# Kernel tuning notes

Measured on AMD Instinct MI355X. Metric: run time of the kernel, lower is better.

## Reference

```python
import jax, jax.numpy as jnp
import numpy as np

B, N, E, H = 8, 2000, 20, 128


def setup_inputs() -> dict:
    key = jax.random.key(0)
    ks = jax.random.split(key, 9)
    s = 1.0 / np.sqrt(H)
    return {
        "x": jax.random.normal(ks[0], (B, N, H), dtype=jnp.float32),
        "e": jax.random.normal(ks[1], (B, N * E, H), dtype=jnp.float32),
        "Wu": jax.random.uniform(ks[2], (H, H), jnp.float32, -s, s),
        "bu": jax.random.uniform(ks[3], (H,), jnp.float32, -s, s),
        "Wv": jax.random.uniform(ks[4], (H, H), jnp.float32, -s, s),
        "bv": jax.random.uniform(ks[5], (H,), jnp.float32, -s, s),
        "We": jax.random.uniform(ks[6], (H, H), jnp.float32, -s, s),
        "be": jax.random.uniform(ks[7], (H,), jnp.float32, -s, s),
        "edge_index": jax.random.randint(ks[8], (B, N * E), 0, N, dtype=jnp.int32),
        "n_edges": E,
    }


def reference(x, e, Wu, bu, Wv, bv, We, be, edge_index, n_edges):
    b, n, h = x.shape
    Ux = x @ Wu + bu                      # [B, N, H] node self-embedding
    Vx = x @ Wv + bv                      # [B, N, H] neighbor embedding
    Ve = e @ We + be                      # [B, N*E, H] edge embedding
    # softmax over the n_edges axis per (node, channel)
    Ve = jax.nn.softmax(Ve.reshape(b, n, n_edges, h), axis=2)
    # gather neighbor features along node axis via edge_index
    Vx_g = jnp.take_along_axis(Vx, edge_index[..., None], axis=1)  # [B, N*E, H]
    to = (Ve * Vx_g.reshape(b, n, n_edges, h)).sum(axis=2)          # [B, N, H]
    return Ux + to
```

## Files before the change

### kernel.cpp

```cpp
#include <hip/hip_runtime.h>

#define B_   8
#define NN   2000
#define EE   20
#define HH   128
#define BN   (B_*NN)
#define NE   (NN*EE)

typedef unsigned short ushort_t;
typedef __bf16 bf16x8 __attribute__((ext_vector_type(8)));
typedef float  f32x4  __attribute__((ext_vector_type(4)));
typedef float  f4     __attribute__((ext_vector_type(4)));
typedef unsigned short us8 __attribute__((ext_vector_type(8)));
typedef unsigned short us4 __attribute__((ext_vector_type(4)));

union FragU { us8 u; bf16x8 b; };
union Frag32 { unsigned int w[4]; us8 u; bf16x8 b; };

__device__ __forceinline__ float b2f(ushort_t v) {
    union { unsigned int i; float f; } c; c.i = ((unsigned int)v) << 16; return c.f;
}
__device__ __forceinline__ ushort_t f2b(float f) {
    union { float f; unsigned int i; } c; c.f = f;
    unsigned int r = (c.i + 0x7FFFu + ((c.i >> 16) & 1u)) >> 16;
    return (ushort_t)r;
}

__global__ __launch_bounds__(256) void k1_embed(
    const float* __restrict__ x,
    const float* __restrict__ Wu, const float* __restrict__ bu,
    const float* __restrict__ Wv, const float* __restrict__ bv,
    ushort_t* __restrict__ Uxb, ushort_t* __restrict__ Vxb)
{
    const int tid  = threadIdx.x;
    const int lane = tid & 63;
    const int wave = tid >> 6;
    const int wm = wave >> 1, wn = wave & 1;
    const int q  = lane >> 4, ln = lane & 15;
    const int m0 = blockIdx.x * 64;
    const int sel = blockIdx.y;
    const float* W    = sel ? Wv : Wu;
    const float* bias = sel ? bv : bu;
    ushort_t* dst = sel ? Vxb : Uxb;

    FragU af[2][4];
#pragma unroll
    for (int tm = 0; tm < 2; ++tm)
#pragma unroll
        for (int ki = 0; ki < 4; ++ki) {
            const float* p = x + (size_t)(m0 + wm * 32 + tm * 16 + ln) * HH + ki * 32 + q * 8;
            f4 lo = *(const f4*)(p);
            f4 hi = *(const f4*)(p + 4);
            us8 t;
#pragma unroll
            for (int r = 0; r < 4; ++r) { t[r] = f2b(lo[r]); t[r + 4] = f2b(hi[r]); }
            af[tm][ki].u = t;
        }

    FragU bf[4][4];
#pragma unroll
    for (int ki = 0; ki < 4; ++ki)
#pragma unroll
        for (int tn = 0; tn < 4; ++tn) {
            int n = wn * 64 + tn * 16 + ln;
            us8 t;
#pragma unroll
            for (int i = 0; i < 8; ++i) t[i] = f2b(W[(ki * 32 + q * 8 + i) * HH + n]);
            bf[ki][tn].u = t;
        }

    f32x4 acc[2][4];
#pragma unroll
    for (int tm = 0; tm < 2; ++tm)
#pragma unroll
        for (int tn = 0; tn < 4; ++tn) acc[tm][tn] = (f32x4){0.f, 0.f, 0.f, 0.f};

#pragma unroll
    for (int ki = 0; ki < 4; ++ki)
#pragma unroll
        for (int tm = 0; tm < 2; ++tm)
#pragma unroll
            for (int tn = 0; tn < 4; ++tn)
                acc[tm][tn] = __builtin_amdgcn_mfma_f32_16x16x32_bf16(
                    af[tm][ki].b, bf[ki][tn].b, acc[tm][tn], 0, 0, 0);

#pragma unroll
    for (int tn = 0; tn < 4; ++tn) {
        int col = wn * 64 + tn * 16 + ln;
        float bb = bias[col];
#pragma unroll
        for (int tm = 0; tm < 2; ++tm) {
            int rowb = m0 + wm * 32 + tm * 16 + q * 4;
#pragma unroll
            for (int r = 0; r < 4; ++r)
                dst[(size_t)(rowb + r) * HH + col] = f2b(acc[tm][tn][r] + bb);
        }
    }
}

#define CSTR 84

__global__ __launch_bounds__(256, 4) void k2_fused(
    const float* __restrict__ e, const float* __restrict__ We,
    const int* __restrict__ eidx,
    const ushort_t* __restrict__ Uxb, const ushort_t* __restrict__ Vxb,
    float* __restrict__ out)
{
    __shared__ __align__(16) unsigned char smem[40960];

    const int tid  = threadIdx.x;
    const int lane = tid & 63;
    const int wave = tid >> 6;
    const int q  = lane >> 4, ln = lane & 15;

    const int b   = blockIdx.y;
    const int nl0 = blockIdx.x * 4;
    const size_t erow0 = (size_t)b * NE + (size_t)nl0 * EE;

    {
        const int rl = lane >> 5;
        const int sl = lane & 31;
#pragma unroll
        for (int i = 0; i < 10; ++i) {
            const int r0 = wave * 20 + 2 * i;
            const int r  = r0 + rl;
            const int ss = sl ^ (r & 7);
            const float* gp = e + (erow0 + r) * (size_t)HH + (ss << 2);
            __builtin_amdgcn_global_load_lds(
                (const __attribute__((address_space(1))) void*)gp,
                (__attribute__((address_space(3))) void*)(smem + r0 * 512),
                16, 0, 0);
        }
    }

    FragU bfr[4][2];
#pragma unroll
    for (int ki = 0; ki < 4; ++ki)
#pragma unroll
        for (int tn = 0; tn < 2; ++tn) {
            int n = wave * 32 + tn * 16 + ln;
            us8 t;
#pragma unroll
            for (int i = 0; i < 8; ++i) t[i] = f2b(We[(ki * 32 + q * 8 + i) * HH + n]);
            bfr[ki][tn].u = t;
        }

    f32x4 acc[5][2];
#pragma unroll
    for (int tm = 0; tm < 5; ++tm)
#pragma unroll
        for (int tn = 0; tn < 2; ++tn) acc[tm][tn] = (f32x4){0.f, 0.f, 0.f, 0.f};

    asm volatile("s_waitcnt vmcnt(0)" ::: "memory");
    __syncthreads();

    const float* As = (const float*)smem;
#pragma unroll
    for (int ki = 0; ki < 4; ++ki) {
        Frag32 af[5];
#pragma unroll
        for (int tm = 0; tm < 5; ++tm) {
            const int r  = tm * 16 + ln;
            const int sw = r & 7;
            const int s0 = ki * 8 + q * 2;
            f4 lo = *(const f4*)(As + r * 128 + ((s0    ) ^ sw) * 4);
            f4 hi = *(const f4*)(As + r * 128 + ((s0 + 1) ^ sw) * 4);
            asm("v_cvt_pk_bf16_f32 %0, %1, %2" : "=v"(af[tm].w[0]) : "v"(lo[0]), "v"(lo[1]));
            asm("v_cvt_pk_bf16_f32 %0, %1, %2" : "=v"(af[tm].w[1]) : "v"(lo[2]), "v"(lo[3]));
            asm("v_cvt_pk_bf16_f32 %0, %1, %2" : "=v"(af[tm].w[2]) : "v"(hi[0]), "v"(hi[1]));
            asm("v_cvt_pk_bf16_f32 %0, %1, %2" : "=v"(af[tm].w[3]) : "v"(hi[2]), "v"(hi[3]));
        }
#pragma unroll
        for (int tm = 0; tm < 5; ++tm)
#pragma unroll
            for (int tn = 0; tn < 2; ++tn)
                acc[tm][tn] = __builtin_amdgcn_mfma_f32_16x16x32_bf16(
                    af[tm].b, bfr[ki][tn].b, acc[tm][tn], 0, 0, 0);
    }

    __syncthreads();

    int* sidx = (int*)(smem + 38400);
    if (tid < 80) sidx[tid] = eidx[erow0 + tid];

    ushort_t* CT = (ushort_t*)smem;
#pragma unroll
    for (int tm = 0; tm < 5; ++tm)
#pragma unroll
        for (int tn = 0; tn < 2; ++tn) {
            int col  = wave * 32 + tn * 16 + ln;
            int rowb = tm * 16 + q * 4;
            us4 pk;
#pragma unroll
            for (int r = 0; r < 4; ++r) pk[r] = f2b(acc[tm][tn][r]);
            *(us4*)(&CT[col * CSTR + rowb]) = pk;
        }

    __syncthreads();

    const int h  = tid & 127;
    const int gp = tid >> 7;
#pragma unroll 1
    for (int j = 0; j < 2; ++j) {
        int g = gp + 2 * j;
        const ushort_t* ctp = &CT[h * CSTR + g * 20];
        float lv[20];
#pragma unroll
        for (int i = 0; i < 5; ++i) {
            us4 v = *(const us4*)(ctp + i * 4);
#pragma unroll
            for (int r = 0; r < 4; ++r) lv[i * 4 + r] = b2f(v[r]);
        }
        float mx = lv[0];
#pragma unroll
        for (int k = 1; k < EE; ++k) mx = fmaxf(mx, lv[k]);

        ushort_t gv[20];
        const int ib = g * 20;
#pragma unroll
        for (int k = 0; k < EE; ++k)
            gv[k] = Vxb[(size_t)(b * NN + sidx[ib + k]) * HH + h];

        float s = 0.f, a = 0.f;
#pragma unroll
        for (int k = 0; k < EE; ++k) {
            float p = __expf(lv[k] - mx);
            s += p;
            a = fmaf(p, b2f(gv[k]), a);
        }
        size_t orow = (size_t)(b * NN + nl0 + g) * HH + h;
        out[orow] = b2f(Uxb[orow]) + a / s;
    }
}

extern "C" void kernel_launch(void* const* d_in, const int* in_sizes, int n_in,
                              void* d_out, int out_size, void* d_ws, size_t ws_size,
                              hipStream_t stream) {
    const float* x  = (const float*)d_in[0];
    const float* e  = (const float*)d_in[1];
    const float* Wu = (const float*)d_in[2];
    const float* bu = (const float*)d_in[3];
    const float* Wv = (const float*)d_in[4];
    const float* bv = (const float*)d_in[5];
    const float* We = (const float*)d_in[6];
    const int*   eidx = (const int*)d_in[8];

    ushort_t* Uxb = (ushort_t*)d_ws;
    ushort_t* Vxb = (ushort_t*)((char*)d_ws + (size_t)BN * HH * 2);
    float*    o   = (float*)d_out;

    k1_embed<<<dim3(250, 2), 256, 0, stream>>>(x, Wu, bu, Wv, bv, Uxb, Vxb);
    k2_fused<<<dim3(500, 8), 256, 0, stream>>>(e, We, eidx, Uxb, Vxb, o);
}
```

Baseline: 267.2 us.

## Load edge tiles directly from global into registers, shrink LDS footprint

The edge-feature tile is now read by every wave straight from global memory into MFMA A-fragments instead of being staged through LDS with global_load_lds and a swizzle. LDS drops to the transposed output buffer plus the index array, and one barrier plus the vmcnt wait are removed. Each wave still reads the whole 80x128 tile itself, so global/L2 traffic for the tile rises about fourfold, with reuse left to the cache. The launch bound is lowered to 3 blocks per SIMD, presumably to give the compiler more registers for the in-flight loads.

```diff
diff --git a/kernel.cpp b/kernel.cpp
--- a/kernel.cpp
+++ b/kernel.cpp
@@ -100,13 +100,14 @@
 
 #define CSTR 84
 
-__global__ __launch_bounds__(256, 4) void k2_fused(
+__global__ __launch_bounds__(256, 3) void k2_fused(
     const float* __restrict__ e, const float* __restrict__ We,
     const int* __restrict__ eidx,
     const ushort_t* __restrict__ Uxb, const ushort_t* __restrict__ Vxb,
     float* __restrict__ out)
 {
-    __shared__ __align__(16) unsigned char smem[40960];
+    __shared__ __align__(16) ushort_t CT[128 * CSTR];
+    __shared__ int sidx[80];
 
     const int tid  = threadIdx.x;
     const int lane = tid & 63;
@@ -117,21 +118,7 @@
     const int nl0 = blockIdx.x * 4;
     const size_t erow0 = (size_t)b * NE + (size_t)nl0 * EE;
 
-    {
-        const int rl = lane >> 5;
-        const int sl = lane & 31;
-#pragma unroll
-        for (int i = 0; i < 10; ++i) {
-            const int r0 = wave * 20 + 2 * i;
-            const int r  = r0 + rl;
-            const int ss = sl ^ (r & 7);
-            const float* gp = e + (erow0 + r) * (size_t)HH + (ss << 2);
-            __builtin_amdgcn_global_load_lds(
-                (const __attribute__((address_space(1))) void*)gp,
-                (__attribute__((address_space(3))) void*)(smem + r0 * 512),
-                16, 0, 0);
-        }
-    }
+    if (tid < 80) sidx[tid] = eidx[erow0 + tid];
 
     FragU bfr[4][2];
 #pragma unroll
@@ -151,20 +138,15 @@
 #pragma unroll
         for (int tn = 0; tn < 2; ++tn) acc[tm][tn] = (f32x4){0.f, 0.f, 0.f, 0.f};
 
-    asm volatile("s_waitcnt vmcnt(0)" ::: "memory");
-    __syncthreads();
-
-    const float* As = (const float*)smem;
+    const float* ap = e + (erow0 + ln) * (size_t)HH + q * 8;
 #pragma unroll
     for (int ki = 0; ki < 4; ++ki) {
         Frag32 af[5];
 #pragma unroll
         for (int tm = 0; tm < 5; ++tm) {
-            const int r  = tm * 16 + ln;
-            const int sw = r & 7;
-            const int s0 = ki * 8 + q * 2;
-            f4 lo = *(const f4*)(As + r * 128 + ((s0    ) ^ sw) * 4);
-            f4 hi = *(const f4*)(As + r * 128 + ((s0 + 1) ^ sw) * 4);
+            const float* p = ap + tm * 16 * HH + ki * 32;
+            f4 lo = *(const f4*)(p);
+            f4 hi = *(const f4*)(p + 4);
             asm("v_cvt_pk_bf16_f32 %0, %1, %2" : "=v"(af[tm].w[0]) : "v"(lo[0]), "v"(lo[1]));
             asm("v_cvt_pk_bf16_f32 %0, %1, %2" : "=v"(af[tm].w[1]) : "v"(lo[2]), "v"(lo[3]));
             asm("v_cvt_pk_bf16_f32 %0, %1, %2" : "=v"(af[tm].w[2]) : "v"(hi[0]), "v"(hi[1]));
@@ -178,12 +160,6 @@
                     af[tm].b, bfr[ki][tn].b, acc[tm][tn], 0, 0, 0);
     }
 
-    __syncthreads();
-
-    int* sidx = (int*)(smem + 38400);
-    if (tid < 80) sidx[tid] = eidx[erow0 + tid];
-
-    ushort_t* CT = (ushort_t*)smem;
 #pragma unroll
     for (int tm = 0; tm < 5; ++tm)
 #pragma unroll
```

After: 315.9 us. 18.2% more time.

## Make edge kernel persistent over 8 node groups with double-buffered LDS prefetch

Applied to the files above, without the earlier changes.

The fused edge kernel now launches 500 blocks, and each block loops over 8 consecutive node groups. While it computes the current group, it prefetches the next group's edge tile into a second LDS buffer via global_load_lds. The We fragments are loaded once per block instead of once per group. The cost is doubled LDS (80KB), lower occupancy (launch bounds 2), and manual vmcnt waits that must match the issued load counts.

```diff
diff --git a/kernel.cpp b/kernel.cpp
--- a/kernel.cpp
+++ b/kernel.cpp
@@ -99,39 +99,43 @@
 }
 
 #define CSTR 84
-
-__global__ __launch_bounds__(256, 4) void k2_fused(
+#define GPB  8
+
+__global__ __launch_bounds__(256, 2) void k2_fused(
     const float* __restrict__ e, const float* __restrict__ We,
     const int* __restrict__ eidx,
     const ushort_t* __restrict__ Uxb, const ushort_t* __restrict__ Vxb,
     float* __restrict__ out)
 {
-    __shared__ __align__(16) unsigned char smem[40960];
+    __shared__ __align__(16) unsigned char smem[2][40960];
 
     const int tid  = threadIdx.x;
     const int lane = tid & 63;
     const int wave = tid >> 6;
     const int q  = lane >> 4, ln = lane & 15;
-
-    const int b   = blockIdx.y;
-    const int nl0 = blockIdx.x * 4;
-    const size_t erow0 = (size_t)b * NE + (size_t)nl0 * EE;
-
-    {
-        const int rl = lane >> 5;
-        const int sl = lane & 31;
+    const int rl = lane >> 5;
+    const int sl = lane & 31;
+
+    const int g0 = blockIdx.x * GPB;
+
+    auto stage = [&](int g, int buf) {
+        const int gb = g / 500;
+        const int gl = g - gb * 500;
+        const size_t er0 = (size_t)gb * NE + (size_t)gl * 80;
 #pragma unroll
         for (int i = 0; i < 10; ++i) {
             const int r0 = wave * 20 + 2 * i;
             const int r  = r0 + rl;
             const int ss = sl ^ (r & 7);
-            const float* gp = e + (erow0 + r) * (size_t)HH + (ss << 2);
+            const float* gp = e + (er0 + r) * (size_t)HH + (ss << 2);
             __builtin_amdgcn_global_load_lds(
                 (const __attribute__((address_space(1))) void*)gp,
-                (__attribute__((address_space(3))) void*)(smem + r0 * 512),
+                (__attribute__((address_space(3))) void*)(&smem[buf][r0 * 512]),
                 16, 0, 0);
         }
-    }
+    };
+
+    stage(g0, 0);
 
     FragU bfr[4][2];
 #pragma unroll
@@ -145,91 +149,111 @@
             bfr[ki][tn].u = t;
         }
 
-    f32x4 acc[5][2];
-#pragma unroll
-    for (int tm = 0; tm < 5; ++tm)
-#pragma unroll
-        for (int tn = 0; tn < 2; ++tn) acc[tm][tn] = (f32x4){0.f, 0.f, 0.f, 0.f};
-
-    asm volatile("s_waitcnt vmcnt(0)" ::: "memory");
-    __syncthreads();
-
-    const float* As = (const float*)smem;
-#pragma unroll
-    for (int ki = 0; ki < 4; ++ki) {
-        Frag32 af[5];
-#pragma unroll
-        for (int tm = 0; tm < 5; ++tm) {
-            const int r  = tm * 16 + ln;
-            const int sw = r & 7;
-            const int s0 = ki * 8 + q * 2;
-            f4 lo = *(const f4*)(As + r * 128 + ((s0    ) ^ sw) * 4);
-            f4 hi = *(const f4*)(As + r * 128 + ((s0 + 1) ^ sw) * 4);
-            asm("v_cvt_pk_bf16_f32 %0, %1, %2" : "=v"(af[tm].w[0]) : "v"(lo[0]), "v"(lo[1]));
-            asm("v_cvt_pk_bf16_f32 %0, %1, %2" : "=v"(af[tm].w[1]) : "v"(lo[2]), "v"(lo[3]));
-            asm("v_cvt_pk_bf16_f32 %0, %1, %2" : "=v"(af[tm].w[2]) : "v"(hi[0]), "v"(hi[1]));
-            asm("v_cvt_pk_bf16_f32 %0, %1, %2" : "=v"(af[tm].w[3]) : "v"(hi[2]), "v"(hi[3]));
-        }
+    int cur = 0;
+#pragma unroll 1
+    for (int t = 0; t < GPB; ++t) {
+        const int g  = g0 + t;
+        const int gb = g / 500;
+        const int gl = g - gb * 500;
+        const int nl0 = gl * 4;
+        const size_t erow0 = (size_t)gb * NE + (size_t)nl0 * EE;
+
+        int ridx = 0;
+        if (tid < 80) ridx = eidx[erow0 + tid];
+
+        if (t + 1 < GPB) stage(g + 1, cur ^ 1);
+
+        if (t == 0)             asm volatile("s_waitcnt vmcnt(10)" ::: "memory");
+        else if (t + 1 < GPB)   asm volatile("s_waitcnt vmcnt(12)" ::: "memory");
+        else                    asm volatile("s_waitcnt vmcnt(2)"  ::: "memory");
+        __builtin_amdgcn_s_barrier();
+
+        const float* As = (const float*)smem[cur];
+        f32x4 acc[5][2];
 #pragma unroll
         for (int tm = 0; tm < 5; ++tm)
 #pragma unroll
-            for (int tn = 0; tn < 2; ++tn)
-                acc[tm][tn] = __builtin_amdgcn_mfma_f32_16x16x32_bf16(
-                    af[tm].b, bfr[ki][tn].b, acc[tm][tn], 0, 0, 0);
-    }
-
-    __syncthreads();
-
-    int* sidx = (int*)(smem + 38400);
-    if (tid < 80) sidx[tid] = eidx[erow0 + tid];
-
-    ushort_t* CT = (ushort_t*)smem;
-#pragma unroll
-    for (int tm = 0; tm < 5; ++tm)
-#pragma unroll
-        for (int tn = 0; tn < 2; ++tn) {
-            int col  = wave * 32 + tn * 16 + ln;
-            int rowb = tm * 16 + q * 4;
-            us4 pk;
-#pragma unroll
-            for (int r = 0; r < 4; ++r) pk[r] = f2b(acc[tm][tn][r]);
-            *(us4*)(&CT[col * CSTR + rowb]) = pk;
-        }
-
-    __syncthreads();
-
-    const int h  = tid & 127;
-    const int gp = tid >> 7;
+            for (int tn = 0; tn < 2; ++tn) acc[tm][tn] = (f32x4){0.f, 0.f, 0.f, 0.f};
+
+#pragma unroll
+        for (int ki = 0; ki < 4; ++ki) {
+            Frag32 af[5];
+#pragma unroll
+            for (int tm = 0; tm < 5; ++tm) {
+                const int r  = tm * 16 + ln;
+                const int sw = r & 7;
+                const int s0 = ki * 8 + q * 2;
+                f4 lo = *(const f4*)(As + r * 128 + ((s0    ) ^ sw) * 4);
+                f4 hi = *(const f4*)(As + r * 128 + ((s0 + 1) ^ sw) * 4);
+                asm("v_cvt_pk_bf16_f32 %0, %1, %2" : "=v"(af[tm].w[0]) : "v"(lo[0]), "v"(lo[1]));
+                asm("v_cvt_pk_bf16_f32 %0, %1, %2" : "=v"(af[tm].w[1]) : "v"(lo[2]), "v"(lo[3]));
+                asm("v_cvt_pk_bf16_f32 %0, %1, %2" : "=v"(af[tm].w[2]) : "v"(hi[0]), "v"(hi[1]));
+                asm("v_cvt_pk_bf16_f32 %0, %1, %2" : "=v"(af[tm].w[3]) : "v"(hi[2]), "v"(hi[3]));
+            }
+#pragma unroll
+            for (int tm = 0; tm < 5; ++tm)
+#pragma unroll
+                for (int tn = 0; tn < 2; ++tn)
+                    acc[tm][tn] = __builtin_amdgcn_mfma_f32_16x16x32_bf16(
+                        af[tm].b, bfr[ki][tn].b, acc[tm][tn], 0, 0, 0);
+        }
+
+        __builtin_amdgcn_s_barrier();
+
+        ushort_t* CT   = (ushort_t*)smem[cur];
+        int*      sidx = (int*)(&smem[cur][38400]);
+        if (tid < 80) sidx[tid] = ridx;
+#pragma unroll
+        for (int tm = 0; tm < 5; ++tm)
+#pragma unroll
+            for (int tn = 0; tn < 2; ++tn) {
+                int col  = wave * 32 + tn * 16 + ln;
+                int rowb = tm * 16 + q * 4;
+                us4 pk;
+#pragma unroll
+                for (int r = 0; r < 4; ++r) pk[r] = f2b(acc[tm][tn][r]);
+                *(us4*)(&CT[col * CSTR + rowb]) = pk;
+            }
+
+        asm volatile("s_waitcnt lgkmcnt(0)" ::: "memory");
+        __builtin_amdgcn_s_barrier();
+
+        const int h  = tid & 127;
+        const int gp = tid >> 7;
 #pragma unroll 1
-    for (int j = 0; j < 2; ++j) {
-        int g = gp + 2 * j;
-        const ushort_t* ctp = &CT[h * CSTR + g * 20];
-        float lv[20];
-#pragma unroll
-        for (int i = 0; i < 5; ++i) {
-            us4 v = *(const us4*)(ctp + i * 4);
-#pragma unroll
-            for (int r = 0; r < 4; ++r) lv[i * 4 + r] = b2f(v[r]);
-        }
-        float mx = lv[0];
-#pragma unroll
-        for (int k = 1; k < EE; ++k) mx = fmaxf(mx, lv[k]);
-
-        ushort_t gv[20];
-        const int ib = g * 20;
-#pragma unroll
-        for (int k = 0; k < EE; ++k)
-            gv[k] = Vxb[(size_t)(b * NN + sidx[ib + k]) * HH + h];
-
-        float s = 0.f, a = 0.f;
-#pragma unroll
-        for (int k = 0; k < EE; ++k) {
-            float p = __expf(lv[k] - mx);
-            s += p;
-            a = fmaf(p, b2f(gv[k]), a);
-        }
-        size_t orow = (size_t)(b * NN + nl0 + g) * HH + h;
-        out[orow] = b2f(Uxb[orow]) + a / s;
+        for (int j = 0; j < 2; ++j) {
+            int gg = gp + 2 * j;
+            const ushort_t* ctp = &CT[h * CSTR + gg * 20];
+            float lv[20];
+#pragma unroll
+            for (int i = 0; i < 5; ++i) {
+                us4 v = *(const us4*)(ctp + i * 4);
+#pragma unroll
+                for (int r = 0; r < 4; ++r) lv[i * 4 + r] = b2f(v[r]);
+            }
+            float mx = lv[0];
+#pragma unroll
+            for (int k = 1; k < EE; ++k) mx = fmaxf(mx, lv[k]);
+
+            ushort_t gv[20];
+            const int ib = gg * 20;
+#pragma unroll
+            for (int k = 0; k < EE; ++k)
+                gv[k] = Vxb[(size_t)(gb * NN + sidx[ib + k]) * HH + h];
+
+            float s = 0.f, a = 0.f;
+#pragma unroll
+            for (int k = 0; k < EE; ++k) {
+                float p = __expf(lv[k] - mx);
+                s += p;
+                a = fmaf(p, b2f(gv[k]), a);
+            }
+            size_t orow = (size_t)(gb * NN + nl0 + gg) * HH + h;
+            out[orow] = b2f(Uxb[orow]) + a / s;
+        }
+
+        __builtin_amdgcn_s_barrier();
+        cur ^= 1;
     }
 }
 
@@ -250,5 +274,5 @@
     float*    o   = (float*)d_out;
 
     k1_embed<<<dim3(250, 2), 256, 0, stream>>>(x, Wu, bu, Wv, bv, Uxb, Vxb);
-    k2_fused<<<dim3(500, 8), 256, 0, stream>>>(e, We, eidx, Uxb, Vxb, o);
-}
+    k2_fused<<<dim3(500), 256, 0, stream>>>(e, We, eidx, Uxb, Vxb, o);
+}
```

New measurement: 268.1 us. About the same (+0.3%).
